# Kernel optimization log

Measured on AMD Instinct MI355X. Metric: run time of the kernel, lower is better.

## Reference

```python
import jax, jax.numpy as jnp
import numpy as np

WS = 7  # window size
SS = 3  # shift size
NH = 3  # heads
EPS = 1e-5


def _layernorm(x, g, b):
    m = jnp.mean(x, axis=-1, keepdims=True)
    v = jnp.mean(jnp.square(x - m), axis=-1, keepdims=True)
    return (x - m) * jax.lax.rsqrt(v + EPS) * g + b


def _rel_index(ws):
    coords = np.stack(np.meshgrid(np.arange(ws), np.arange(ws), indexing='ij'))
    cf = coords.reshape(2, -1)
    rel = (cf[:, :, None] - cf[:, None, :]).transpose(1, 2, 0)
    rel[:, :, 0] += ws - 1
    rel[:, :, 1] += ws - 1
    rel[:, :, 0] *= 2 * ws - 1
    return rel.sum(-1)  # [ws*ws, ws*ws]


def _shift_mask(H, W, ws, ss):
    img = np.zeros((H, W), np.int32)
    cnt = 0
    for hs in (slice(0, -ws), slice(-ws, -ss), slice(-ss, None)):
        for wsl in (slice(0, -ws), slice(-ws, -ss), slice(-ss, None)):
            img[hs, wsl] = cnt
            cnt += 1
    mw = img.reshape(H // ws, ws, W // ws, ws).transpose(0, 2, 1, 3).reshape(-1, ws * ws)
    diff = mw[:, None, :] - mw[:, :, None]
    return np.where(diff != 0, -100.0, 0.0).astype(np.float32)  # [nW, N, N]


def setup_inputs() -> dict:
    key = jax.random.key(0)
    ks = jax.random.split(key, 8)
    B, H, W, C = 64, 56, 56, 96
    hid = 4 * C
    s = 0.02
    return {
        'x': jax.random.normal(ks[0], (B, H * W, C), jnp.float32),
        'attn_mask': jnp.asarray(_shift_mask(H, W, WS, SS)),
        'ln1_g': jnp.ones((C,), jnp.float32),
        'ln1_b': jnp.zeros((C,), jnp.float32),
        'qkv_w': jax.random.normal(ks[1], (3 * C, C), jnp.float32) * s,
        'qkv_b': jnp.zeros((3 * C,), jnp.float32),
        'rel_bias_table': jax.random.normal(ks[2], ((2 * WS - 1) ** 2, NH), jnp.float32) * s,
        'rel_index': jnp.asarray(_rel_index(WS), jnp.int64) if jax.config.jax_enable_x64 else jnp.asarray(_rel_index(WS), jnp.int32),
        'proj_w': jax.random.normal(ks[3], (C, C), jnp.float32) * s,
        'proj_b': jnp.zeros((C,), jnp.float32),
        'ln2_g': jnp.ones((C,), jnp.float32),
        'ln2_b': jnp.zeros((C,), jnp.float32),
        'fc1_w': jax.random.normal(ks[4], (hid, C), jnp.float32) * s,
        'fc1_b': jnp.zeros((hid,), jnp.float32),
        'fc2_w': jax.random.normal(ks[5], (C, hid), jnp.float32) * s,
        'fc2_b': jnp.zeros((C,), jnp.float32),
        'H': H,
        'W': W,
    }


def reference(x, attn_mask, ln1_g, ln1_b, qkv_w, qkv_b, rel_bias_table, rel_index,
              proj_w, proj_b, ln2_g, ln2_b, fc1_w, fc1_b, fc2_w, fc2_b, H, W):
    B, L, C = x.shape
    ws, ss, nh = WS, SS, NH
    hd = C // nh
    N = ws * ws
    nW = (H // ws) * (W // ws)

    shortcut = x
    h = _layernorm(x, ln1_g, ln1_b).reshape(B, H, W, C)
    # cyclic shift (H,W divisible by ws -> no padding needed)
    h = jnp.roll(h, shift=(-ss, -ss), axis=(1, 2))
    # window partition: [B, H, W, C] -> [B*nW, N, C]
    h = h.reshape(B, H // ws, ws, W // ws, ws, C).transpose(0, 1, 3, 2, 4, 5)
    xw = h.reshape(B * nW, N, C)

    # qkv projection
    qkv = xw @ qkv_w.T + qkv_b                     # [B_, N, 3C]
    qkv = qkv.reshape(B * nW, N, 3, nh, hd).transpose(2, 0, 3, 1, 4)
    q, k, v = qkv[0], qkv[1], qkv[2]               # [B_, nh, N, hd]
    scale = hd ** (-0.5)
    attn = jnp.einsum('bhnd,bhmd->bhnm', q * scale, k)   # [B_, nh, N, N]

    bias = rel_bias_table[rel_index.reshape(-1)].reshape(N, N, nh)
    attn = attn + bias.transpose(2, 0, 1)[None]

    # shifted-window mask: [nW, N, N] broadcast over batch and heads
    attn = attn.reshape(B, nW, nh, N, N) + attn_mask[None, :, None]
    attn = jax.nn.softmax(attn.reshape(B * nW, nh, N, N), axis=-1)

    out = jnp.einsum('bhnm,bhmd->bhnd', attn, v)   # [B_, nh, N, hd]
    out = out.transpose(0, 2, 1, 3).reshape(B * nW, N, C)
    out = out @ proj_w.T + proj_b

    # window reverse + reverse shift
    out = out.reshape(B, H // ws, W // ws, ws, ws, C).transpose(0, 1, 3, 2, 4, 5).reshape(B, H, W, C)
    out = jnp.roll(out, shift=(ss, ss), axis=(1, 2)).reshape(B, H * W, C)

    h = shortcut + out
    # MLP block
    m = _layernorm(h, ln2_g, ln2_b)
    m = jax.nn.gelu(m @ fc1_w.T + fc1_b, approximate=False)
    m = m @ fc2_w.T + fc2_b
    return h + m
```

## Files before the change

### kernel.cpp

```cpp
#include <hip/hip_runtime.h>
#include <math.h>


#define CDIM 96
#define SCALE_QK 0.17677669529663687f

typedef __attribute__((ext_vector_type(8))) short bf16x8;
typedef __attribute__((ext_vector_type(4))) float f32x4;
typedef __attribute__((ext_vector_type(2))) unsigned int u32x2;
typedef __attribute__((ext_vector_type(4))) unsigned int u32x4;

__device__ inline unsigned short f2b(float f) {
    union { float f; unsigned u; } v; v.f = f;
    unsigned r = v.u + 0x7FFF + ((v.u >> 16) & 1);
    return (unsigned short)(r >> 16);
}
__device__ inline unsigned pkcvt(float a, float b) {
    unsigned d;
    asm("v_cvt_pk_bf16_f32 %0, %1, %2" : "=v"(d) : "v"(a), "v"(b));
    return d;
}
__device__ inline float bitsf(unsigned u) {
    union { unsigned u; float f; } v; v.u = u; return v.f;
}
__device__ inline bf16x8 mk8(unsigned d0, unsigned d1, unsigned d2, unsigned d3) {
    union { u32x4 u; bf16x8 h; } v;
    v.u = (u32x4){d0, d1, d2, d3};
    return v.h;
}
__device__ inline bf16x8 sel8(bool c, bf16x8 a, bf16x8 b) {
    union { bf16x8 h; u32x4 u; } A, B, R;
    A.h = a; B.h = b;
    R.u.x = c ? A.u.x : B.u.x;
    R.u.y = c ? A.u.y : B.u.y;
    R.u.z = c ? A.u.z : B.u.z;
    R.u.w = c ? A.u.w : B.u.w;
    return R.h;
}

__global__ __launch_bounds__(256) void conv_w_kernel(
    const float* __restrict__ qkv_w, const float* __restrict__ proj_w,
    const float* __restrict__ fc1_w, const float* __restrict__ fc2_w,
    unsigned short* __restrict__ ws)
{
    const int i = blockIdx.x * 256 + threadIdx.x;
    if (i < 27648)       ws[i] = f2b(qkv_w[i]);
    else if (i < 36864)  ws[i] = f2b(proj_w[i - 27648]);
    else if (i < 73728)  ws[i] = f2b(fc1_w[i - 36864]);
    else if (i < 110592) ws[i] = f2b(fc2_w[i - 73728]);
}

__global__ __launch_bounds__(256) void build_bmfrag_kernel(
    const float* __restrict__ attn_mask, const float* __restrict__ rel_bias_table,
    const int* __restrict__ rel_index, unsigned short* __restrict__ bmf)
{
    const int i = blockIdx.x * 256 + threadIdx.x;
    const int lane = i & 63;
    const int mt = (i >> 6) & 3;
    const int kt = (i >> 8) & 3;
    const int t3 = i >> 10;
    const int h = t3 % 3, widx = t3 / 3;
    const int q = mt * 16 + (lane & 15);
    const int kb = kt * 16 + (lane >> 4) * 4;
    float vv[4];
    #pragma unroll
    for (int rr = 0; rr < 4; ++rr) {
        const int k = kb + rr;
        float val = -1.0e30f;
        if (q < 49 && k < 49) {
            const int idx = q * 49 + k;
            val = rel_bias_table[rel_index[idx] * 3 + h] + attn_mask[widx * 2401 + idx];
        }
        vv[rr] = val;
    }
    u32x2 pw;
    pw.x = (unsigned)f2b(vv[0]) | ((unsigned)f2b(vv[1]) << 16);
    pw.y = (unsigned)f2b(vv[2]) | ((unsigned)f2b(vv[3]) << 16);
    *(u32x2*)(bmf + (size_t)i * 4) = pw;
}

__global__ __launch_bounds__(64, 2) void swin_fused(
    const float* __restrict__ x,
    const float* __restrict__ ln1_g, const float* __restrict__ ln1_b,
    const float* __restrict__ qkv_b, const float* __restrict__ proj_b,
    const float* __restrict__ ln2_g, const float* __restrict__ ln2_b,
    const float* __restrict__ fc1_b, const float* __restrict__ fc2_b,
    const unsigned short* __restrict__ wqkv,
    const unsigned short* __restrict__ wproj,
    const unsigned short* __restrict__ wfc1,
    const unsigned short* __restrict__ wfc2,
    const unsigned short* __restrict__ bmfrag,
    float* __restrict__ out)
{
    __shared__ __align__(16) unsigned short smem[49][104];
    __shared__ __align__(16) unsigned scx[4][16][20];
    unsigned short (*xt)[104]  = smem;
    unsigned short (*kss)[104] = smem;

    const int w = blockIdx.x, b = w >> 6, widx = w & 63;
    const int wi = widx >> 3, wj = widx & 7;
    const int lane = threadIdx.x;
    const int l15 = lane & 15, gq = lane >> 4;
    const int lk = gq * 8, g4 = gq * 4;

    #define XCHG(dst, slot, p00, p01, p10, p11)                                   \
        {                                                                          \
            unsigned* row_ = &scx[slot][l15][0];                                   \
            *(u32x2*)(row_ + gq * 2)     = (u32x2){(p00), (p01)};                  \
            *(u32x2*)(row_ + 8 + gq * 2) = (u32x2){(p10), (p11)};                  \
            (dst) = *(const bf16x8*)(row_ + gq * 4);                               \
        }

    size_t xrow[4];
    #pragma unroll
    for (int mt = 0; mt < 4; ++mt) {
        const int tok = mt * 16 + l15;
        const int p = tok / 7, qq = tok - 7 * p;
        int sr = wi * 7 + p + 3;   if (sr >= 56) sr -= 56;
        int scl = wj * 7 + qq + 3; if (scl >= 56) scl -= 56;
        xrow[mt] = ((size_t)b * 3136 + (size_t)(sr * 56 + scl)) * CDIM;
    }

    {
        const int n = lane;
        if (n < 49) {
            const int p = n / 7, qq = n - 7 * p;
            int sr = wi * 7 + p + 3;   if (sr >= 56) sr -= 56;
            int scl = wj * 7 + qq + 3; if (scl >= 56) scl -= 56;
            const float* xr = x + ((size_t)b * 3136 + (size_t)(sr * 56 + scl)) * CDIM;
            float s = 0.f, ss2 = 0.f;
            #pragma unroll
            for (int i = 0; i < 24; ++i) {
                const float4 f = *(const float4*)(xr + i * 4);
                s += f.x + f.y + f.z + f.w;
                ss2 += f.x*f.x + f.y*f.y + f.z*f.z + f.w*f.w;
            }
            const float mean = s * (1.f / 96.f);
            const float rstd = rsqrtf(ss2 * (1.f / 96.f) - mean * mean + 1e-5f);
            #pragma unroll
            for (int i = 0; i < 12; ++i) {
                const float4 f0 = *(const float4*)(xr + i * 8);
                const float4 f1 = *(const float4*)(xr + i * 8 + 4);
                const float4 g0 = *(const float4*)(ln1_g + i * 8);
                const float4 g1 = *(const float4*)(ln1_g + i * 8 + 4);
                const float4 b0 = *(const float4*)(ln1_b + i * 8);
                const float4 b1 = *(const float4*)(ln1_b + i * 8 + 4);
                u32x4 pv;
                pv.x = pkcvt((f0.x-mean)*rstd*g0.x + b0.x, (f0.y-mean)*rstd*g0.y + b0.y);
                pv.y = pkcvt((f0.z-mean)*rstd*g0.z + b0.z, (f0.w-mean)*rstd*g0.w + b0.w);
                pv.z = pkcvt((f1.x-mean)*rstd*g1.x + b1.x, (f1.y-mean)*rstd*g1.y + b1.y);
                pv.w = pkcvt((f1.z-mean)*rstd*g1.z + b1.z, (f1.w-mean)*rstd*g1.w + b1.w);
                *(u32x4*)&xt[n][i * 8] = pv;
            }
        }
    }

    bf16x8 bx[4][3];
    #pragma unroll
    for (int mt = 0; mt < 3; ++mt)
        #pragma unroll
        for (int c = 0; c < 3; ++c)
            bx[mt][c] = *(const bf16x8*)&xt[mt * 16 + l15][c * 32 + lk];
    {
        const bool valid = (l15 == 0);
        #pragma unroll
        for (int c = 0; c < 3; ++c) {
            const bf16x8 ld = *(const bf16x8*)&xt[48][c * 32 + lk];
            const bf16x8 z = {};
            bx[3][c] = sel8(valid, ld, z);
        }
    }

    bf16x8 qfrag[4][3];
    #pragma unroll
    for (int c = 0; c < 3; ++c) {
        const unsigned short* wr0 = wqkv + (size_t)((2*c) * 16 + l15) * 96;
        const unsigned short* wr1 = wqkv + (size_t)((2*c+1) * 16 + l15) * 96;
        bf16x8 wA[3], wB[3];
        #pragma unroll
        for (int i = 0; i < 3; ++i) {
            wA[i] = *(const bf16x8*)(wr0 + i * 32 + lk);
            wB[i] = *(const bf16x8*)(wr1 + i * 32 + lk);
        }
        const float4 qb0 = *(const float4*)(qkv_b + (2*c) * 16 + g4);
        const float4 qb1 = *(const float4*)(qkv_b + (2*c+1) * 16 + g4);
        #pragma unroll
        for (int mt = 0; mt < 4; ++mt) {
            f32x4 aA = {0.f,0.f,0.f,0.f}, aB = {0.f,0.f,0.f,0.f};
            #pragma unroll
            for (int i = 0; i < 3; ++i) {
                aA = __builtin_amdgcn_mfma_f32_16x16x32_bf16(wA[i], bx[mt][i], aA, 0, 0, 0);
                aB = __builtin_amdgcn_mfma_f32_16x16x32_bf16(wB[i], bx[mt][i], aB, 0, 0, 0);
            }
            const unsigned pk00 = pkcvt((aA[0] + qb0.x) * SCALE_QK, (aA[1] + qb0.y) * SCALE_QK);
            const unsigned pk01 = pkcvt((aA[2] + qb0.z) * SCALE_QK, (aA[3] + qb0.w) * SCALE_QK);
            const unsigned pk10 = pkcvt((aB[0] + qb1.x) * SCALE_QK, (aB[1] + qb1.y) * SCALE_QK);
            const unsigned pk11 = pkcvt((aB[2] + qb1.z) * SCALE_QK, (aB[3] + qb1.w) * SCALE_QK);
            XCHG(qfrag[mt][c], mt, pk00, pk01, pk10, pk11);
        }
    }

    bf16x8 vfrag[6][2];
    #pragma unroll
    for (int vf = 0; vf < 6; ++vf) {
        const unsigned short* wr = wqkv + (size_t)(192 + vf * 16 + l15) * 96;
        bf16x8 wV[3];
        #pragma unroll
        for (int i = 0; i < 3; ++i) wV[i] = *(const bf16x8*)(wr + i * 32 + lk);
        const float bias = qkv_b[192 + vf * 16 + l15];
        f32x4 a[4];
        #pragma unroll
        for (int mt = 0; mt < 4; ++mt) {
            f32x4 acc = {0.f,0.f,0.f,0.f};
            #pragma unroll
            for (int i = 0; i < 3; ++i)
                acc = __builtin_amdgcn_mfma_f32_16x16x32_bf16(bx[mt][i], wV[i], acc, 0, 0, 0);
            a[mt] = acc;
        }
        #pragma unroll
        for (int tc = 0; tc < 2; ++tc) {
            const unsigned pk00 = pkcvt(a[2*tc][0] + bias, a[2*tc][1] + bias);
            const unsigned pk01 = pkcvt(a[2*tc][2] + bias, a[2*tc][3] + bias);
            const unsigned pk10 = pkcvt(a[2*tc+1][0] + bias, a[2*tc+1][1] + bias);
            const unsigned pk11 = pkcvt(a[2*tc+1][2] + bias, a[2*tc+1][3] + bias);
            XCHG(vfrag[vf][tc], ((vf * 2 + tc) & 3), pk00, pk01, pk10, pk11);
        }
    }

    #pragma unroll 1
    for (int t = 0; t < 6; ++t) {
        const unsigned short* wr = wqkv + (size_t)((6 + t) * 16 + l15) * 96;
        bf16x8 wK[3];
        #pragma unroll
        for (int i = 0; i < 3; ++i) wK[i] = *(const bf16x8*)(wr + i * 32 + lk);
        const float4 kb4 = *(const float4*)(qkv_b + (6 + t) * 16 + g4);
        #pragma unroll
        for (int mt = 0; mt < 4; ++mt) {
            f32x4 acc = {0.f,0.f,0.f,0.f};
            #pragma unroll
            for (int i = 0; i < 3; ++i)
                acc = __builtin_amdgcn_mfma_f32_16x16x32_bf16(wK[i], bx[mt][i], acc, 0, 0, 0);
            const int tok = mt * 16 + l15;
            if (tok < 49) {
                u32x2 pw;
                pw.x = pkcvt(acc[0] + kb4.x, acc[1] + kb4.y);
                pw.y = pkcvt(acc[2] + kb4.z, acc[3] + kb4.w);
                *(u32x2*)&kss[tok][t * 16 + g4] = pw;
            }
        }
    }

    bf16x8 bxA[4][3];
    #pragma unroll
    for (int h = 0; h < 3; ++h) {
        bf16x8 kb8;
        {
            const float4 kb0 = *(const float4*)(qkv_b + 96 + h * 32 + lk);
            const float4 kb1 = *(const float4*)(qkv_b + 96 + h * 32 + lk + 4);
            kb8 = mk8(pkcvt(kb0.x, kb0.y), pkcvt(kb0.z, kb0.w),
                      pkcvt(kb1.x, kb1.y), pkcvt(kb1.z, kb1.w));
        }
        bf16x8 ak[4];
        #pragma unroll
        for (int kt = 0; kt < 3; ++kt)
            ak[kt] = *(const bf16x8*)&kss[kt * 16 + l15][h * 32 + lk];
        {
            const bf16x8 ld48 = *(const bf16x8*)&kss[48][h * 32 + lk];
            ak[3] = sel8(l15 == 0, ld48, kb8);
        }
        #pragma unroll
        for (int mt = 0; mt < 4; ++mt) {
            const unsigned short* bmb = bmfrag + (size_t)(widx * 3 + h) * 4096 + mt * 256;
            f32x4 s[4];
            #pragma unroll
            for (int kt = 0; kt < 4; ++kt) {
                const u32x2 cw = *(const u32x2*)(bmb + kt * 1024 + lane * 4);
                f32x4 c;
                c[0] = bitsf(cw.x << 16); c[1] = bitsf(cw.x & 0xffff0000u);
                c[2] = bitsf(cw.y << 16); c[3] = bitsf(cw.y & 0xffff0000u);
                s[kt] = __builtin_amdgcn_mfma_f32_16x16x32_bf16(ak[kt], qfrag[mt][h], c, 0, 0, 0);
            }
            float mx = s[0][0];
            #pragma unroll
            for (int kt = 0; kt < 4; ++kt)
                #pragma unroll
                for (int rr = 0; rr < 4; ++rr) mx = fmaxf(mx, s[kt][rr]);
            mx = fmaxf(mx, __shfl_xor(mx, 16));
            mx = fmaxf(mx, __shfl_xor(mx, 32));
            float sum = 0.f;
            #pragma unroll
            for (int kt = 0; kt < 4; ++kt)
                #pragma unroll
                for (int rr = 0; rr < 4; ++rr) {
                    const float e = __expf(s[kt][rr] - mx);
                    s[kt][rr] = e; sum += e;
                }
            sum += __shfl_xor(sum, 16);
            sum += __shfl_xor(sum, 32);
            const float inv = __fdividef(1.0f, sum);
            const unsigned pk00 = pkcvt(s[0][0], s[0][1]), pk01 = pkcvt(s[0][2], s[0][3]);
            const unsigned pk10 = pkcvt(s[1][0], s[1][1]), pk11 = pkcvt(s[1][2], s[1][3]);
            const unsigned pk20 = pkcvt(s[2][0], s[2][1]), pk21 = pkcvt(s[2][2], s[2][3]);
            const unsigned pk30 = pkcvt(s[3][0], s[3][1]), pk31 = pkcvt(s[3][2], s[3][3]);
            bf16x8 pb0, pb1;
            XCHG(pb0, 0, pk00, pk01, pk10, pk11);
            XCHG(pb1, 1, pk20, pk21, pk30, pk31);
            f32x4 o0 = {0.f,0.f,0.f,0.f}, o1 = {0.f,0.f,0.f,0.f};
            o0 = __builtin_amdgcn_mfma_f32_16x16x32_bf16(vfrag[h*2][0],   pb0, o0, 0, 0, 0);
            o0 = __builtin_amdgcn_mfma_f32_16x16x32_bf16(vfrag[h*2][1],   pb1, o0, 0, 0, 0);
            o1 = __builtin_amdgcn_mfma_f32_16x16x32_bf16(vfrag[h*2+1][0], pb0, o1, 0, 0, 0);
            o1 = __builtin_amdgcn_mfma_f32_16x16x32_bf16(vfrag[h*2+1][1], pb1, o1, 0, 0, 0);
            const unsigned q00 = pkcvt(o0[0] * inv, o0[1] * inv);
            const unsigned q01 = pkcvt(o0[2] * inv, o0[3] * inv);
            const unsigned q10 = pkcvt(o1[0] * inv, o1[1] * inv);
            const unsigned q11 = pkcvt(o1[2] * inv, o1[3] * inv);
            XCHG(bxA[mt][h], 2, q00, q01, q10, q11);
        }
    }

    f32x4 hacc[4][6];
    #pragma unroll
    for (int ct = 0; ct < 6; ++ct) {
        const unsigned short* wr = wproj + (size_t)(ct * 16 + l15) * 96;
        bf16x8 wp[3];
        #pragma unroll
        for (int i = 0; i < 3; ++i) wp[i] = *(const bf16x8*)(wr + i * 32 + lk);
        const float4 pb4 = *(const float4*)(proj_b + ct * 16 + g4);
        #pragma unroll
        for (int mt = 0; mt < 4; ++mt) {
            f32x4 acc = {0.f,0.f,0.f,0.f};
            #pragma unroll
            for (int i = 0; i < 3; ++i)
                acc = __builtin_amdgcn_mfma_f32_16x16x32_bf16(wp[i], bxA[mt][i], acc, 0, 0, 0);
            const float4 xv = *(const float4*)(x + xrow[mt] + ct * 16 + g4);
            hacc[mt][ct][0] = acc[0] + pb4.x + xv.x;
            hacc[mt][ct][1] = acc[1] + pb4.y + xv.y;
            hacc[mt][ct][2] = acc[2] + pb4.z + xv.z;
            hacc[mt][ct][3] = acc[3] + pb4.w + xv.w;
        }
    }

    bf16x8 mbx[4][3];
    #pragma unroll
    for (int mt = 0; mt < 4; ++mt) {
        float s = 0.f, ss2 = 0.f;
        #pragma unroll
        for (int ct = 0; ct < 6; ++ct)
            #pragma unroll
            for (int rr = 0; rr < 4; ++rr) { s += hacc[mt][ct][rr]; ss2 += hacc[mt][ct][rr] * hacc[mt][ct][rr]; }
        s += __shfl_xor(s, 16);  ss2 += __shfl_xor(ss2, 16);
        s += __shfl_xor(s, 32);  ss2 += __shfl_xor(ss2, 32);
        const float mean = s * (1.f / 96.f);
        const float rstd = rsqrtf(ss2 * (1.f / 96.f) - mean * mean + 1e-5f);
        #pragma unroll
        for (int kc = 0; kc < 3; ++kc) {
            const float4 g0 = *(const float4*)(ln2_g + (2*kc) * 16 + g4);
            const float4 b0 = *(const float4*)(ln2_b + (2*kc) * 16 + g4);
            const float4 g1 = *(const float4*)(ln2_g + (2*kc+1) * 16 + g4);
            const float4 b1 = *(const float4*)(ln2_b + (2*kc+1) * 16 + g4);
            const float* g0p = &g0.x; const float* b0p = &b0.x;
            const float* g1p = &g1.x; const float* b1p = &b1.x;
            float v0[4], v1[4];
            #pragma unroll
            for (int rr = 0; rr < 4; ++rr) {
                v0[rr] = (hacc[mt][2*kc][rr]   - mean) * rstd * g0p[rr] + b0p[rr];
                v1[rr] = (hacc[mt][2*kc+1][rr] - mean) * rstd * g1p[rr] + b1p[rr];
            }
            const unsigned pk00 = pkcvt(v0[0], v0[1]), pk01 = pkcvt(v0[2], v0[3]);
            const unsigned pk10 = pkcvt(v1[0], v1[1]), pk11 = pkcvt(v1[2], v1[3]);
            XCHG(mbx[mt][kc], kc, pk00, pk01, pk10, pk11);
        }
    }
    #pragma unroll
    for (int ct = 0; ct < 6; ++ct) {
        const float4 b2v = *(const float4*)(fc2_b + ct * 16 + g4);
        #pragma unroll
        for (int mt = 0; mt < 4; ++mt) {
            hacc[mt][ct][0] += b2v.x; hacc[mt][ct][1] += b2v.y;
            hacc[mt][ct][2] += b2v.z; hacc[mt][ct][3] += b2v.w;
        }
    }

    #pragma unroll 1
    for (int kc = 0; kc < 12; ++kc) {
        const int hb = kc * 32;
        const unsigned short* w0 = wfc1 + (size_t)(hb + l15) * 96;
        const unsigned short* w1 = wfc1 + (size_t)(hb + 16 + l15) * 96;
        bf16x8 w0f[3], w1f[3];
        #pragma unroll
        for (int i = 0; i < 3; ++i) {
            w0f[i] = *(const bf16x8*)(w0 + i * 32 + lk);
            w1f[i] = *(const bf16x8*)(w1 + i * 32 + lk);
        }
        const float4 bv0 = *(const float4*)(fc1_b + hb + g4);
        const float4 bv1 = *(const float4*)(fc1_b + hb + 16 + g4);
        const float* b0p = &bv0.x; const float* b1p = &bv1.x;
        bf16x8 pb[4];
        #pragma unroll
        for (int mt = 0; mt < 4; ++mt) {
            f32x4 s0 = {0.f,0.f,0.f,0.f}, s1 = {0.f,0.f,0.f,0.f};
            #pragma unroll
            for (int i = 0; i < 3; ++i) {
                s0 = __builtin_amdgcn_mfma_f32_16x16x32_bf16(w0f[i], mbx[mt][i], s0, 0, 0, 0);
                s1 = __builtin_amdgcn_mfma_f32_16x16x32_bf16(w1f[i], mbx[mt][i], s1, 0, 0, 0);
            }
            float ge0[4], ge1[4];
            #pragma unroll
            for (int rr = 0; rr < 4; ++rr) {
                float u = s0[rr] + b0p[rr];
                float u2 = u * u;
                float n2y = u * (-1.5957691216f - 0.0713548162f * u2);
                ge0[rr] = __fdividef(u, 1.f + __expf(n2y));
                u = s1[rr] + b1p[rr];
                u2 = u * u;
                n2y = u * (-1.5957691216f - 0.0713548162f * u2);
                ge1[rr] = __fdividef(u, 1.f + __expf(n2y));
            }
            const unsigned pk00 = pkcvt(ge0[0], ge0[1]), pk01 = pkcvt(ge0[2], ge0[3]);
            const unsigned pk10 = pkcvt(ge1[0], ge1[1]), pk11 = pkcvt(ge1[2], ge1[3]);
            XCHG(pb[mt], mt, pk00, pk01, pk10, pk11);
        }
        #pragma unroll
        for (int ct = 0; ct < 6; ++ct) {
            const bf16x8 w2f = *(const bf16x8*)(wfc2 + (size_t)(ct * 16 + l15) * 384 + hb + lk);
            #pragma unroll
            for (int mt = 0; mt < 4; ++mt)
                hacc[mt][ct] = __builtin_amdgcn_mfma_f32_16x16x32_bf16(w2f, pb[mt], hacc[mt][ct], 0, 0, 0);
        }
    }

    #pragma unroll
    for (int mt = 0; mt < 4; ++mt) {
        const int tok = mt * 16 + l15;
        if (tok < 49) {
            float* ob = out + xrow[mt];
            #pragma unroll
            for (int ct = 0; ct < 6; ++ct) {
                float4 o4;
                o4.x = hacc[mt][ct][0]; o4.y = hacc[mt][ct][1];
                o4.z = hacc[mt][ct][2]; o4.w = hacc[mt][ct][3];
                *(float4*)(ob + ct * 16 + g4) = o4;
            }
        }
    }
    #undef XCHG
}

extern "C" void kernel_launch(void* const* d_in, const int* in_sizes, int n_in,
                              void* d_out, int out_size, void* d_ws, size_t ws_size,
                              hipStream_t stream) {
    (void)n_in; (void)out_size; (void)ws_size;
    const float* x        = (const float*)d_in[0];
    const float* attn_msk = (const float*)d_in[1];
    const float* ln1_g    = (const float*)d_in[2];
    const float* ln1_b    = (const float*)d_in[3];
    const float* qkv_w    = (const float*)d_in[4];
    const float* qkv_b    = (const float*)d_in[5];
    const float* rel_tab  = (const float*)d_in[6];
    const int*   rel_idx  = (const int*)d_in[7];
    const float* proj_w   = (const float*)d_in[8];
    const float* proj_b   = (const float*)d_in[9];
    const float* ln2_g    = (const float*)d_in[10];
    const float* ln2_b    = (const float*)d_in[11];
    const float* fc1_w    = (const float*)d_in[12];
    const float* fc1_b    = (const float*)d_in[13];
    const float* fc2_w    = (const float*)d_in[14];
    const float* fc2_b    = (const float*)d_in[15];
    float* out = (float*)d_out;
    unsigned short* wsb = (unsigned short*)d_ws;
    unsigned short* bmf = wsb + 110592;

    const int B = in_sizes[0] / (3136 * 96);

    conv_w_kernel<<<(110592 + 255) / 256, 256, 0, stream>>>(qkv_w, proj_w, fc1_w, fc2_w, wsb);
    build_bmfrag_kernel<<<196608 / 256, 256, 0, stream>>>(attn_msk, rel_tab, rel_idx, bmf);

    swin_fused<<<B * 64, 64, 0, stream>>>(
        x, ln1_g, ln1_b, qkv_b, proj_b, ln2_g, ln2_b, fc1_b, fc2_b,
        wsb, wsb + 27648, wsb + 36864, wsb + 73728, bmf, out);
}
```

Before: 185.4 us.

## Double-buffer MLP weight tiles into LDS with async global_load_lds prefetch

Replaces the per-iteration direct global loads of fc1/fc2 weight fragments in the MLP loop with asynchronous global_load_lds transfers into a two-stage LDS buffer. The next chunk's tiles are issued before computing on the current one, with explicit vmcnt waits, so weight fetch latency is meant to overlap MFMA and GELU work. The cost is about 24 KB of extra LDS per block, which may reduce occupancy, and the manual vmcnt counting is fragile: the fc1_b bias loads are also vector-memory ops, so the waits have to account for them too.

```diff
diff --git a/kernel.cpp b/kernel.cpp
--- a/kernel.cpp
+++ b/kernel.cpp
@@ -94,6 +94,7 @@
 {
     __shared__ __align__(16) unsigned short smem[49][104];
     __shared__ __align__(16) unsigned scx[4][16][20];
+    __shared__ __align__(16) unsigned short wpre[2][12][512];
     unsigned short (*xt)[104]  = smem;
     unsigned short (*kss)[104] = smem;
 
@@ -110,6 +111,12 @@
             *(u32x2*)(row_ + 8 + gq * 2) = (u32x2){(p10), (p11)};                  \
             (dst) = *(const bf16x8*)(row_ + gq * 4);                               \
         }
+
+    #define ISSUE_TILE(bufi, tidx, srcptr)                                         \
+        __builtin_amdgcn_global_load_lds(                                          \
+            (const __attribute__((address_space(1))) unsigned int*)(const void*)(srcptr), \
+            (__attribute__((address_space(3))) unsigned int*)(void*)&wpre[bufi][tidx][0], \
+            16, 0, 0);
 
     size_t xrow[4];
     #pragma unroll
@@ -381,19 +388,44 @@
         }
     }
 
+    {
+        const int hb0 = 0;
+        #pragma unroll
+        for (int i = 0; i < 3; ++i) {
+            ISSUE_TILE(0, i,     wfc1 + (size_t)(hb0 + l15) * 96 + i * 32 + lk);
+            ISSUE_TILE(0, 3 + i, wfc1 + (size_t)(hb0 + 16 + l15) * 96 + i * 32 + lk);
+        }
+        #pragma unroll
+        for (int ct = 0; ct < 6; ++ct)
+            ISSUE_TILE(0, 6 + ct, wfc2 + (size_t)(ct * 16 + l15) * 384 + hb0 + lk);
+    }
     #pragma unroll 1
     for (int kc = 0; kc < 12; ++kc) {
+        const int buf = kc & 1;
         const int hb = kc * 32;
-        const unsigned short* w0 = wfc1 + (size_t)(hb + l15) * 96;
-        const unsigned short* w1 = wfc1 + (size_t)(hb + 16 + l15) * 96;
-        bf16x8 w0f[3], w1f[3];
-        #pragma unroll
-        for (int i = 0; i < 3; ++i) {
-            w0f[i] = *(const bf16x8*)(w0 + i * 32 + lk);
-            w1f[i] = *(const bf16x8*)(w1 + i * 32 + lk);
-        }
         const float4 bv0 = *(const float4*)(fc1_b + hb + g4);
         const float4 bv1 = *(const float4*)(fc1_b + hb + 16 + g4);
+        if (kc < 11) {
+            const int hb1 = hb + 32, nb = buf ^ 1;
+            #pragma unroll
+            for (int i = 0; i < 3; ++i) {
+                ISSUE_TILE(nb, i,     wfc1 + (size_t)(hb1 + l15) * 96 + i * 32 + lk);
+                ISSUE_TILE(nb, 3 + i, wfc1 + (size_t)(hb1 + 16 + l15) * 96 + i * 32 + lk);
+            }
+            #pragma unroll
+            for (int ct = 0; ct < 6; ++ct)
+                ISSUE_TILE(nb, 6 + ct, wfc2 + (size_t)(ct * 16 + l15) * 384 + hb1 + lk);
+            asm volatile("s_waitcnt vmcnt(14)" ::: "memory");
+        } else {
+            asm volatile("s_waitcnt vmcnt(2)" ::: "memory");
+        }
+        __builtin_amdgcn_sched_barrier(0);
+        bf16x8 w0f[3], w1f[3];
+        #pragma unroll
+        for (int i = 0; i < 3; ++i) {
+            w0f[i] = *(const bf16x8*)&wpre[buf][i][lane * 8];
+            w1f[i] = *(const bf16x8*)&wpre[buf][3 + i][lane * 8];
+        }
         const float* b0p = &bv0.x; const float* b1p = &bv1.x;
         bf16x8 pb[4];
         #pragma unroll
@@ -422,7 +454,7 @@
         }
         #pragma unroll
         for (int ct = 0; ct < 6; ++ct) {
-            const bf16x8 w2f = *(const bf16x8*)(wfc2 + (size_t)(ct * 16 + l15) * 384 + hb + lk);
+            const bf16x8 w2f = *(const bf16x8*)&wpre[buf][6 + ct][lane * 8];
             #pragma unroll
             for (int mt = 0; mt < 4; ++mt)
                 hacc[mt][ct] = __builtin_amdgcn_mfma_f32_16x16x32_bf16(w2f, pb[mt], hacc[mt][ct], 0, 0, 0);
@@ -444,6 +476,7 @@
         }
     }
     #undef XCHG
+    #undef ISSUE_TILE
 }
 
 extern "C" void kernel_launch(void* const* d_in, const int* in_sizes, int n_in,
```

After: 230.2 us. 24.2% more time.
